# Performance work log

Measured on AMD Instinct MI355X. Metric: run time of the kernel, lower is better.

The kernel has to match this reference:

```python
import jax, jax.numpy as jnp
import numpy as np
from jax import lax

PAD_IDX = 9182


def setup_inputs() -> dict:
    key = jax.random.key(0)
    ks = jax.random.split(key, 16)
    B, S = 16, 256
    V, E, H, SH = 32000, 512, 1024, 1024
    sc = 0.05
    embed = jax.random.normal(ks[0], (V, E), jnp.float32) * sc
    embed = embed.at[PAD_IDX].set(0.0)  # padding_idx row
    inp = {
        "context_encoding": jax.random.normal(ks[1], (B, 1, SH), jnp.float32),
        "target": jax.random.randint(ks[2], (B, S), 0, V),
        "embed": embed,                                              # embed_in.weight (shared out proj)
        "W_s2d": jax.random.normal(ks[3], (H, SH), jnp.float32) * sc,   # ses_to_dec
        "b_s2d": jax.random.normal(ks[4], (H,), jnp.float32) * sc,
        "W_dec_inf": jax.random.normal(ks[5], (2 * E, H), jnp.float32) * sc,
        "W_ses_inf": jax.random.normal(ks[6], (2 * E, SH), jnp.float32) * sc,
        "W_emb_inf": jax.random.normal(ks[7], (2 * E, E), jnp.float32) * sc,
        "b_emb_inf": jax.random.normal(ks[8], (2 * E,), jnp.float32) * sc,
        "W_ih": jax.random.normal(ks[9], (3 * H, E), jnp.float32) * sc,  # GRU input weights
        "W_hh": jax.random.normal(ks[10], (3 * H, H), jnp.float32) * sc,  # GRU hidden weights
        "b_ih": jax.random.normal(ks[11], (3 * H,), jnp.float32) * sc,
        "b_hh": jax.random.normal(ks[12], (3 * H,), jnp.float32) * sc,
    }
    return inp


def _decode(context_encoding, embed, W_s2d, b_s2d, W_dec_inf, W_ses_inf,
            W_emb_inf, b_emb_inf, W_ih, W_hh, b_ih, b_hh, target):
    B, S = target.shape
    ctx = context_encoding[:, 0]                    # [B, SH]
    ses_inf = ctx @ W_ses_inf.T                     # [B, 2E]
    h0 = jnp.tanh(ctx @ W_s2d.T + b_s2d)            # [B, H] init decoder hidden

    emb = embed[target]                             # [B, S, E]
    emb_inf = emb @ W_emb_inf.T + b_emb_inf         # [B, S, 2E]
    x_proj = emb @ W_ih.T + b_ih                    # [B, S, 3H] precomputed GRU input gates

    def gru_step(h, xp):
        gh = h @ W_hh.T + b_hh                      # [B, 3H]
        xr, xz, xn = jnp.split(xp, 3, axis=-1)
        hr, hz, hn = jnp.split(gh, 3, axis=-1)
        r = jax.nn.sigmoid(xr + hr)
        z = jax.nn.sigmoid(xz + hz)
        n = jnp.tanh(xn + r * hn)
        h_new = (1.0 - z) * n + z * h
        return h_new, h_new

    _, hs = lax.scan(gru_step, h0, jnp.swapaxes(x_proj, 0, 1))  # [S, B, H]
    hs = jnp.swapaxes(hs, 0, 1)                     # [B, S, H]

    total = hs @ W_dec_inf.T + ses_inf[:, None, :] + emb_inf  # [B, S, 2E]
    mx = total.reshape(B, S, -1, 2).max(axis=-1)    # maxout pairs -> [B, S, E]
    logits = mx @ embed.T                           # shared embedding out proj [B, S, V]
    return logits


def reference(context_encoding, target, embed, W_s2d, b_s2d, W_dec_inf,
              W_ses_inf, W_emb_inf, b_emb_inf, W_ih, W_hh, b_ih, b_hh):
    dec_o = _decode(context_encoding, embed, W_s2d, b_s2d, W_dec_inf,
                    W_ses_inf, W_emb_inf, b_emb_inf, W_ih, W_hh, b_ih, b_hh,
                    target)
    return dec_o
```

## Files before the change

### kernel.cpp

```cpp
#include <hip/hip_runtime.h>

typedef unsigned short u16;
typedef unsigned int u32;
typedef __attribute__((ext_vector_type(8))) __bf16 bf16x8;
typedef __attribute__((ext_vector_type(4))) float f32x4;
typedef __attribute__((ext_vector_type(4))) u32 u32x4;

#define ASYNC16(g, l) __builtin_amdgcn_global_load_lds( \
    (const __attribute__((address_space(1))) unsigned int*)(g), \
    (__attribute__((address_space(3))) unsigned int*)(l), 16, 0, 0)

__device__ __forceinline__ u16 f2bf(float f){
  unsigned u = __float_as_uint(f);
  unsigned r = u + 0x7fffu + ((u >> 16) & 1u);
  return (u16)(r >> 16);
}

__global__ __launch_bounds__(256) void f2bf_kernel(const float* __restrict__ in,
                                                   u16* __restrict__ out, int n){
  int i = (blockIdx.x * 256 + threadIdx.x) * 8;
  if (i >= n) return;
  float4 a = *(const float4*)&in[i];
  float4 b = *(const float4*)&in[i + 4];
  u16 r[8] = {f2bf(a.x), f2bf(a.y), f2bf(a.z), f2bf(a.w),
              f2bf(b.x), f2bf(b.y), f2bf(b.z), f2bf(b.w)};
  *(uint4*)&out[i] = *(const uint4*)r;
}

__global__ __launch_bounds__(256) void ctx_kernel(const float* __restrict__ ctx,
    const float* __restrict__ Wses, const float* __restrict__ Ws2d,
    const float* __restrict__ bs2d, float* __restrict__ sesinf,
    float* __restrict__ h0f, u16* __restrict__ h0bf){
  int id = blockIdx.x * 4 + (threadIdx.x >> 6);
  int lane = threadIdx.x & 63;
  int n = id & 1023, b = (id >> 10) & 15, mat = id >> 14;
  const float* w = (mat ? Ws2d : Wses) + (size_t)n * 1024;
  const float* x = ctx + (size_t)b * 1024;
  float v = 0.f;
  #pragma unroll 4
  for (int k = lane; k < 1024; k += 64) v += x[k] * w[k];
  #pragma unroll
  for (int off = 32; off; off >>= 1) v += __shfl_down(v, off);
  if (lane == 0){
    if (mat == 0) sesinf[b * 1024 + n] = v;
    else {
      float t = tanhf(v + bs2d[n]);
      h0f[b * 1024 + n] = t;
      h0bf[b * 1024 + n] = f2bf(t);
    }
  }
}

__global__ void gather_kernel(const int* __restrict__ target,
                              const u16* __restrict__ embedBF, u16* __restrict__ embBF){
  int i = blockIdx.x;
  int t = target[i];
  int lane = threadIdx.x;
  *(uint4*)&embBF[(size_t)i * 512 + lane * 8] =
      *(const uint4*)&embedBF[(size_t)t * 512 + lane * 8];
}

template<int EPI, int SWZ>
__global__ __launch_bounds__(256) void gemm_bt(
    const u16* __restrict__ A, const u16* __restrict__ B, float* __restrict__ C,
    int M, int N, int K,
    const float* __restrict__ bias, const float* __restrict__ add0,
    const float* __restrict__ add1, u16* __restrict__ mxout)
{
  __shared__ u16 sA[2][128 * 32];
  __shared__ u16 sB[2][128 * 32];
  int bx = blockIdx.x, by = blockIdx.y;
  if (SWZ){
    int nwg = gridDim.x * gridDim.y;
    int wg = by * gridDim.x + bx;
    int q = nwg >> 3;
    int nw = (wg & 7) * q + (wg >> 3);
    bx = nw % gridDim.x; by = nw / gridDim.x;
  }
  const int n0 = bx * 128;
  const int m0 = by * 128;
  const int tid = threadIdx.x;
  const int lane = tid & 63;
  const int wid = tid >> 6;
  const int wm = (wid >> 1) * 64, wn = (wid & 1) * 64;
  const int l15 = lane & 15, kg = (lane >> 4) * 8;
  (void)M;

  f32x4 zero = {0.f, 0.f, 0.f, 0.f};
  f32x4 acc[4][4];
  #pragma unroll
  for (int m = 0; m < 4; m++)
    #pragma unroll
    for (int n = 0; n < 4; n++) acc[m][n] = zero;

  auto stage = [&](int buf, int kk){
    const u16* Ab = A + (size_t)m0 * K + kk;
    const u16* Bb = B + (size_t)n0 * K + kk;
    #pragma unroll
    for (int j = 0; j < 2; j++){
      int c = j * 256 + tid;
      ASYNC16(Ab + (size_t)(c >> 2) * K + (c & 3) * 8, &sA[buf][c * 8]);
    }
    #pragma unroll
    for (int j = 0; j < 2; j++){
      int c = j * 256 + tid;
      ASYNC16(Bb + (size_t)(c >> 2) * K + (c & 3) * 8, &sB[buf][c * 8]);
    }
  };

  stage(0, 0);
  int cur = 0;
  for (int kk = 0; kk < K; kk += 32){
    __syncthreads();
    if (kk + 32 < K) stage(cur ^ 1, kk + 32);
    bf16x8 af[4], bf_[4];
    #pragma unroll
    for (int m = 0; m < 4; m++)
      af[m] = *(const bf16x8*)&sA[cur][(wm + m * 16 + l15) * 32 + kg];
    #pragma unroll
    for (int n = 0; n < 4; n++)
      bf_[n] = *(const bf16x8*)&sB[cur][(wn + n * 16 + l15) * 32 + kg];
    #pragma unroll
    for (int m = 0; m < 4; m++)
      #pragma unroll
      for (int n = 0; n < 4; n++)
        acc[m][n] = __builtin_amdgcn_mfma_f32_16x16x32_bf16(af[m], bf_[n], acc[m][n], 0, 0, 0);
    cur ^= 1;
  }

  const int rb = m0 + wm + (lane >> 4) * 4;
  const int cb = n0 + wn + l15;
  #pragma unroll
  for (int m = 0; m < 4; m++){
    #pragma unroll
    for (int n = 0; n < 4; n++){
      #pragma unroll
      for (int i = 0; i < 4; i++){
        int row = rb + m * 16 + i;
        int col = cb + n * 16;
        float v = acc[m][n][i];
        if (EPI == 1) v += bias[col];
        if (EPI == 2 || EPI == 3)
          v += add0[(row >> 8) * N + col] + add1[(size_t)row * N + col];
        if (EPI == 3){
          float w = __shfl_xor(v, 1);
          if ((l15 & 1) == 0)
            mxout[(size_t)row * (N >> 1) + (col >> 1)] = f2bf(fmaxf(v, w));
        } else {
          C[(size_t)row * N + col] = v;
        }
      }
    }
  }
}

#define GRU_NWG 64
#define GRU_LDS 136192

__global__ __launch_bounds__(256) void gru_kernel(
    const u16* __restrict__ WhhBF, const float* __restrict__ bhh,
    const float* __restrict__ xproj, const float* __restrict__ h0f,
    const u16* __restrict__ h0bf, u16* __restrict__ hsBF, int* flags)
{
  extern __shared__ char smem[];
  u16*  Wl   = (u16*)smem;
  u16*  hb   = Wl + 48 * 1032;
  float* gbuf = (float*)(smem + 132096);
  float* hown = gbuf + 3 * 256;

  const int g = blockIdx.x;
  const int j0 = g * 16;
  const int tid = threadIdx.x;
  const int lane = tid & 63;
  const int wid = tid >> 6;
  const int bb = tid >> 4, jj = tid & 15;

  for (int c = tid; c < 48 * 128; c += 256){
    int r = c >> 7, cg = (c & 127) * 8;
    int gate = r >> 4, n = r & 15;
    *(uint4*)&Wl[r * 1032 + cg] =
        *(const uint4*)&WhhBF[(size_t)(gate * 1024 + j0 + n) * 1024 + cg];
  }
  hown[bb * 16 + jj] = h0f[bb * 1024 + j0 + jj];
  const float bh0 = bhh[j0 + jj];
  const float bh1 = bhh[1024 + j0 + jj];
  const float bh2 = bhh[2048 + j0 + jj];
  u32* hs32 = (u32*)hsBF;
  __syncthreads();

  for (int s = 0; s < 256; ++s){
    if (s == 0){
      #pragma unroll
      for (int k = 0; k < 8; k++){
        int c = tid + k * 256;
        int b = c >> 7, cg = (c & 127) * 8;
        *(uint4*)&hb[b * 1032 + cg] = *(const uint4*)&h0bf[b * 1024 + cg];
      }
    } else {
      u32x4 r[8];
      #pragma unroll
      for (int k = 0; k < 8; k++){
        int c = tid + k * 256;
        int b = c >> 7, cg = (c & 127) * 8;
        const u16* src = &hsBF[(size_t)((b << 8) + s - 1) * 1024 + cg];
        asm volatile("global_load_dwordx4 %0, %1, off sc1"
                     : "=v"(r[k]) : "v"(src) : "memory");
      }
      asm volatile("s_waitcnt vmcnt(0)" ::: "memory");
      __builtin_amdgcn_sched_barrier(0);
      #pragma unroll
      for (int k = 0; k < 8; k++){
        int c = tid + k * 256;
        int b = c >> 7, cg = (c & 127) * 8;
        *(u32x4*)&hb[b * 1032 + cg] = r[k];
      }
    }

    const float* xp = xproj + ((size_t)(bb << 8) + s) * 3072;
    float xr = xp[j0 + jj], xz = xp[1024 + j0 + jj], xn = xp[2048 + j0 + jj];
    __syncthreads();

    if (wid < 3){
      f32x4 acc0 = {0.f, 0.f, 0.f, 0.f};
      f32x4 acc1 = {0.f, 0.f, 0.f, 0.f};
      const int l15 = lane & 15, kg = (lane >> 4) * 8;
      const u16* wrow = &Wl[(wid * 16 + l15) * 1032];
      const u16* hrow = &hb[l15 * 1032];
      #pragma unroll 8
      for (int kk = 0; kk < 1024; kk += 64){
        bf16x8 a0 = *(const bf16x8*)&hrow[kk + kg];
        bf16x8 w0 = *(const bf16x8*)&wrow[kk + kg];
        acc0 = __builtin_amdgcn_mfma_f32_16x16x32_bf16(a0, w0, acc0, 0, 0, 0);
        bf16x8 a1 = *(const bf16x8*)&hrow[kk + 32 + kg];
        bf16x8 w1 = *(const bf16x8*)&wrow[kk + 32 + kg];
        acc1 = __builtin_amdgcn_mfma_f32_16x16x32_bf16(a1, w1, acc1, 0, 0, 0);
      }
      #pragma unroll
      for (int i = 0; i < 4; ++i)
        gbuf[wid * 256 + ((lane >> 4) * 4 + i) * 16 + l15] = acc0[i] + acc1[i];
    }
    __syncthreads();

    {
      float hr = gbuf[0 * 256 + bb * 16 + jj] + bh0;
      float hz = gbuf[1 * 256 + bb * 16 + jj] + bh1;
      float hn = gbuf[2 * 256 + bb * 16 + jj] + bh2;
      float r = 1.f / (1.f + __expf(-(xr + hr)));
      float z = 1.f / (1.f + __expf(-(xz + hz)));
      float nn = tanhf(xn + r * hn);
      float hnew = (1.f - z) * nn + z * hown[bb * 16 + jj];
      hown[bb * 16 + jj] = hnew;
      float hnext = __shfl_down(hnew, 1);
      if ((jj & 1) == 0){
        u32 pack = (u32)f2bf(hnew) | ((u32)f2bf(hnext) << 16);
        size_t e = (size_t)((bb << 8) + s) * 1024 + j0 + jj;
        __hip_atomic_store(&hs32[e >> 1], pack, __ATOMIC_RELAXED,
                           __HIP_MEMORY_SCOPE_AGENT);
      }
    }

    if (s < 255){
      asm volatile("s_waitcnt vmcnt(0)" ::: "memory");
      __syncthreads();
      if (tid == 0)
        __hip_atomic_store(&flags[g * 32], s + 1, __ATOMIC_RELAXED,
                           __HIP_MEMORY_SCOPE_AGENT);
      if (wid == 0){
        while (__hip_atomic_load(&flags[lane * 32], __ATOMIC_RELAXED,
                                 __HIP_MEMORY_SCOPE_AGENT) <= s)
          __builtin_amdgcn_s_sleep(1);
      }
      __syncthreads();
    }
  }
}

extern "C" void kernel_launch(void* const* d_in, const int* in_sizes, int n_in,
                              void* d_out, int out_size, void* d_ws, size_t ws_size,
                              hipStream_t stream)
{
  const float* ctx    = (const float*)d_in[0];
  const int*   target = (const int*)d_in[1];
  const float* embed  = (const float*)d_in[2];
  const float* Ws2d   = (const float*)d_in[3];
  const float* bs2d   = (const float*)d_in[4];
  const float* Wdec   = (const float*)d_in[5];
  const float* Wses   = (const float*)d_in[6];
  const float* Wemb   = (const float*)d_in[7];
  const float* bemb   = (const float*)d_in[8];
  const float* Wih    = (const float*)d_in[9];
  const float* Whh    = (const float*)d_in[10];
  const float* bih    = (const float*)d_in[11];
  const float* bhh    = (const float*)d_in[12];
  float* out = (float*)d_out;

  char* ws = (char*)d_ws;
  size_t off = 0;
  auto alloc = [&](size_t bytes)->char*{
    char* p = ws + off; off += (bytes + 255) & ~(size_t)255; return p;
  };
  u16*   embedBF = (u16*)alloc(32000ull * 512 * 2);
  u16*   WihBF   = (u16*)alloc(3072ull * 512 * 2);
  u16*   WembBF  = (u16*)alloc(1024ull * 512 * 2);
  u16*   WdecBF  = (u16*)alloc(1024ull * 1024 * 2);
  u16*   WhhBF   = (u16*)alloc(3072ull * 1024 * 2);
  u16*   embBF   = (u16*)alloc(4096ull * 512 * 2);
  float* xproj   = (float*)alloc(4096ull * 3072 * 4);
  float* embinf  = (float*)alloc(4096ull * 1024 * 4);
  float* sesinf  = (float*)alloc(16ull * 1024 * 4);
  float* h0f     = (float*)alloc(16ull * 1024 * 4);
  u16*   h0bf    = (u16*)alloc(16ull * 1024 * 2);
  u16*   hsBF    = (u16*)alloc(4096ull * 1024 * 2);
  u16*   mxBF    = (u16*)alloc(4096ull * 512 * 2);
  int*   flags   = (int*)alloc(16384);
  (void)ws_size; (void)in_sizes; (void)n_in; (void)out_size;

  hipFuncSetAttribute((const void*)gru_kernel,
                      hipFuncAttributeMaxDynamicSharedMemorySize, GRU_LDS);
  hipMemsetAsync(flags, 0, 16384, stream);

  auto conv = [&](const float* in, u16* o, size_t n){
    f2bf_kernel<<<dim3((unsigned)((n / 8 + 255) / 256)), 256, 0, stream>>>(in, o, (int)n);
  };
  conv(embed, embedBF, 32000ull * 512);
  conv(Wih,   WihBF,   3072ull * 512);
  conv(Wemb,  WembBF,  1024ull * 512);
  conv(Wdec,  WdecBF,  1024ull * 1024);
  conv(Whh,   WhhBF,   3072ull * 1024);

  ctx_kernel<<<8192, 256, 0, stream>>>(ctx, Wses, Ws2d, bs2d, sesinf, h0f, h0bf);
  gather_kernel<<<4096, 64, 0, stream>>>(target, embedBF, embBF);

  gemm_bt<1,0><<<dim3(3072 / 128, 4096 / 128), 256, 0, stream>>>(
      embBF, WihBF, xproj, 4096, 3072, 512, bih, nullptr, nullptr, nullptr);
  gemm_bt<1,0><<<dim3(1024 / 128, 4096 / 128), 256, 0, stream>>>(
      embBF, WembBF, embinf, 4096, 1024, 512, bemb, nullptr, nullptr, nullptr);

  gru_kernel<<<GRU_NWG, 256, GRU_LDS, stream>>>(WhhBF, bhh, xproj, h0f, h0bf, hsBF, flags);

  gemm_bt<3,0><<<dim3(1024 / 128, 4096 / 128), 256, 0, stream>>>(
      hsBF, WdecBF, nullptr, 4096, 1024, 1024, nullptr, sesinf, embinf, mxBF);

  gemm_bt<0,1><<<dim3(32000 / 128, 4096 / 128), 256, 0, stream>>>(
      mxBF, embedBF, out, 4096, 32000, 512, nullptr, nullptr, nullptr, nullptr);
}
```

Before: 1.323 ms.

## Restructure GRU recurrence into 16 large workgroups reading W_hh from global

The persistent GRU kernel drops from 64 workgroups of 256 threads to 16 workgroups of 1024 threads, each owning 64 hidden units instead of 16. The weight slice is no longer staged in LDS; each MFMA wave reads its W_hh rows straight from global memory (cache) at every step. The goal is to cut the number of workgroups in the per-step cross-workgroup flag barrier and the redundant hidden-state loads. The cost is re-reading the weights from L2 every step instead of LDS, and far fewer CUs doing the matvec.

```diff
diff --git a/kernel.cpp b/kernel.cpp
--- a/kernel.cpp
+++ b/kernel.cpp
@@ -154,53 +154,48 @@
   }
 }
 
-#define GRU_NWG 64
-#define GRU_LDS 136192
-
-__global__ __launch_bounds__(256) void gru_kernel(
+#define GRU_NWG 16
+
+__global__ __launch_bounds__(1024) void gru_kernel(
     const u16* __restrict__ WhhBF, const float* __restrict__ bhh,
     const float* __restrict__ xproj, const float* __restrict__ h0f,
     const u16* __restrict__ h0bf, u16* __restrict__ hsBF, int* flags)
 {
-  extern __shared__ char smem[];
-  u16*  Wl   = (u16*)smem;
-  u16*  hb   = Wl + 48 * 1032;
-  float* gbuf = (float*)(smem + 132096);
-  float* hown = gbuf + 3 * 256;
+  __shared__ u16   hb[16 * 1032];
+  __shared__ float gbuf[12 * 256];
+  __shared__ float hown[16 * 64];
 
   const int g = blockIdx.x;
-  const int j0 = g * 16;
+  const int j0 = g * 64;
   const int tid = threadIdx.x;
   const int lane = tid & 63;
   const int wid = tid >> 6;
-  const int bb = tid >> 4, jj = tid & 15;
-
-  for (int c = tid; c < 48 * 128; c += 256){
-    int r = c >> 7, cg = (c & 127) * 8;
-    int gate = r >> 4, n = r & 15;
-    *(uint4*)&Wl[r * 1032 + cg] =
-        *(const uint4*)&WhhBF[(size_t)(gate * 1024 + j0 + n) * 1024 + cg];
-  }
-  hown[bb * 16 + jj] = h0f[bb * 1024 + j0 + jj];
+  const int bb = wid;
+  const int jj = lane;
+  const int l15 = lane & 15, kh = lane >> 4;
+
+  hown[bb * 64 + jj] = h0f[bb * 1024 + j0 + jj];
   const float bh0 = bhh[j0 + jj];
   const float bh1 = bhh[1024 + j0 + jj];
   const float bh2 = bhh[2048 + j0 + jj];
+  const u16* wr = WhhBF +
+      (size_t)((wid >> 2) * 1024 + j0 + (wid & 3) * 16 + l15) * 1024;
   u32* hs32 = (u32*)hsBF;
   __syncthreads();
 
   for (int s = 0; s < 256; ++s){
     if (s == 0){
       #pragma unroll
-      for (int k = 0; k < 8; k++){
-        int c = tid + k * 256;
+      for (int k = 0; k < 2; k++){
+        int c = tid + k * 1024;
         int b = c >> 7, cg = (c & 127) * 8;
         *(uint4*)&hb[b * 1032 + cg] = *(const uint4*)&h0bf[b * 1024 + cg];
       }
     } else {
-      u32x4 r[8];
-      #pragma unroll
-      for (int k = 0; k < 8; k++){
-        int c = tid + k * 256;
+      u32x4 r[2];
+      #pragma unroll
+      for (int k = 0; k < 2; k++){
+        int c = tid + k * 1024;
         int b = c >> 7, cg = (c & 127) * 8;
         const u16* src = &hsBF[(size_t)((b << 8) + s - 1) * 1024 + cg];
         asm volatile("global_load_dwordx4 %0, %1, off sc1"
@@ -209,8 +204,8 @@
       asm volatile("s_waitcnt vmcnt(0)" ::: "memory");
       __builtin_amdgcn_sched_barrier(0);
       #pragma unroll
-      for (int k = 0; k < 8; k++){
-        int c = tid + k * 256;
+      for (int k = 0; k < 2; k++){
+        int c = tid + k * 1024;
         int b = c >> 7, cg = (c & 127) * 8;
         *(u32x4*)&hb[b * 1032 + cg] = r[k];
       }
@@ -220,36 +215,37 @@
     float xr = xp[j0 + jj], xz = xp[1024 + j0 + jj], xn = xp[2048 + j0 + jj];
     __syncthreads();
 
-    if (wid < 3){
+    if (wid < 12){
       f32x4 acc0 = {0.f, 0.f, 0.f, 0.f};
       f32x4 acc1 = {0.f, 0.f, 0.f, 0.f};
-      const int l15 = lane & 15, kg = (lane >> 4) * 8;
-      const u16* wrow = &Wl[(wid * 16 + l15) * 1032];
+      const int kh8 = kh * 8;
       const u16* hrow = &hb[l15 * 1032];
-      #pragma unroll 8
+      #pragma unroll 4
       for (int kk = 0; kk < 1024; kk += 64){
-        bf16x8 a0 = *(const bf16x8*)&hrow[kk + kg];
-        bf16x8 w0 = *(const bf16x8*)&wrow[kk + kg];
+        bf16x8 a0 = *(const bf16x8*)&hrow[kk + kh8];
+        bf16x8 w0 = *(const bf16x8*)&wr[kk + kh8];
         acc0 = __builtin_amdgcn_mfma_f32_16x16x32_bf16(a0, w0, acc0, 0, 0, 0);
-        bf16x8 a1 = *(const bf16x8*)&hrow[kk + 32 + kg];
-        bf16x8 w1 = *(const bf16x8*)&wrow[kk + 32 + kg];
+        bf16x8 a1 = *(const bf16x8*)&hrow[kk + 32 + kh8];
+        bf16x8 w1 = *(const bf16x8*)&wr[kk + 32 + kh8];
         acc1 = __builtin_amdgcn_mfma_f32_16x16x32_bf16(a1, w1, acc1, 0, 0, 0);
       }
       #pragma unroll
       for (int i = 0; i < 4; ++i)
-        gbuf[wid * 256 + ((lane >> 4) * 4 + i) * 16 + l15] = acc0[i] + acc1[i];
+        gbuf[wid * 256 + (kh * 4 + i) * 16 + l15] = acc0[i] + acc1[i];
     }
     __syncthreads();
 
     {
-      float hr = gbuf[0 * 256 + bb * 16 + jj] + bh0;
-      float hz = gbuf[1 * 256 + bb * 16 + jj] + bh1;
-      float hn = gbuf[2 * 256 + bb * 16 + jj] + bh2;
+      int tc = (jj >> 4);
+      int ic = bb * 16 + (jj & 15);
+      float hr = gbuf[(0 * 4 + tc) * 256 + ic] + bh0;
+      float hz = gbuf[(1 * 4 + tc) * 256 + ic] + bh1;
+      float hn = gbuf[(2 * 4 + tc) * 256 + ic] + bh2;
       float r = 1.f / (1.f + __expf(-(xr + hr)));
       float z = 1.f / (1.f + __expf(-(xz + hz)));
       float nn = tanhf(xn + r * hn);
-      float hnew = (1.f - z) * nn + z * hown[bb * 16 + jj];
-      hown[bb * 16 + jj] = hnew;
+      float hnew = (1.f - z) * nn + z * hown[bb * 64 + jj];
+      hown[bb * 64 + jj] = hnew;
       float hnext = __shfl_down(hnew, 1);
       if ((jj & 1) == 0){
         u32 pack = (u32)f2bf(hnew) | ((u32)f2bf(hnext) << 16);
@@ -265,7 +261,7 @@
       if (tid == 0)
         __hip_atomic_store(&flags[g * 32], s + 1, __ATOMIC_RELAXED,
                            __HIP_MEMORY_SCOPE_AGENT);
-      if (wid == 0){
+      if (wid == 0 && lane < GRU_NWG){
         while (__hip_atomic_load(&flags[lane * 32], __ATOMIC_RELAXED,
                                  __HIP_MEMORY_SCOPE_AGENT) <= s)
           __builtin_amdgcn_s_sleep(1);
@@ -315,8 +311,6 @@
   int*   flags   = (int*)alloc(16384);
   (void)ws_size; (void)in_sizes; (void)n_in; (void)out_size;
 
-  hipFuncSetAttribute((const void*)gru_kernel,
-                      hipFuncAttributeMaxDynamicSharedMemorySize, GRU_LDS);
   hipMemsetAsync(flags, 0, 16384, stream);
 
   auto conv = [&](const float* in, u16* o, size_t n){
@@ -336,7 +330,7 @@
   gemm_bt<1,0><<<dim3(1024 / 128, 4096 / 128), 256, 0, stream>>>(
       embBF, WembBF, embinf, 4096, 1024, 512, bemb, nullptr, nullptr, nullptr);
 
-  gru_kernel<<<GRU_NWG, 256, GRU_LDS, stream>>>(WhhBF, bhh, xproj, h0f, h0bf, hsBF, flags);
+  gru_kernel<<<GRU_NWG, 1024, 0, stream>>>(WhhBF, bhh, xproj, h0f, h0bf, hsBF, flags);
 
   gemm_bt<3,0><<<dim3(1024 / 128, 4096 / 128), 256, 0, stream>>>(
       hsBF, WdecBF, nullptr, 4096, 1024, 1024, nullptr, sesinf, embinf, mxBF);
```

Measured after the change: 3.676 ms. +177.8%, slower.

## Split GRU recurrent matvec K dimension across 12 waves per block

Applied to the files above, without the earlier changes.

The GRU kernel now launches 1024 threads per block instead of 256. The per-step hidden-state matvec splits K=1024 into four chunks, so 12 waves each compute one gate and one K quarter. Partial sums land in a larger gbuf and are reduced by the first 256 threads before the gate math. This shortens the serial MFMA chain on the latency-bound recurrence, at the cost of extra LDS, more partial-sum reads and heavier block-wide barriers.

```diff
diff --git a/kernel.cpp b/kernel.cpp
--- a/kernel.cpp
+++ b/kernel.cpp
@@ -155,9 +155,9 @@
 }
 
 #define GRU_NWG 64
-#define GRU_LDS 136192
-
-__global__ __launch_bounds__(256) void gru_kernel(
+#define GRU_LDS 145408
+
+__global__ __launch_bounds__(1024) void gru_kernel(
     const u16* __restrict__ WhhBF, const float* __restrict__ bhh,
     const float* __restrict__ xproj, const float* __restrict__ h0f,
     const u16* __restrict__ h0bf, u16* __restrict__ hsBF, int* flags)
@@ -166,41 +166,45 @@
   u16*  Wl   = (u16*)smem;
   u16*  hb   = Wl + 48 * 1032;
   float* gbuf = (float*)(smem + 132096);
-  float* hown = gbuf + 3 * 256;
+  float* hown = gbuf + 12 * 256;
 
   const int g = blockIdx.x;
   const int j0 = g * 16;
   const int tid = threadIdx.x;
   const int lane = tid & 63;
   const int wid = tid >> 6;
-  const int bb = tid >> 4, jj = tid & 15;
-
-  for (int c = tid; c < 48 * 128; c += 256){
+  const int l15 = lane & 15, kh8 = (lane >> 4) * 8;
+
+  for (int c = tid; c < 48 * 128; c += 1024){
     int r = c >> 7, cg = (c & 127) * 8;
     int gate = r >> 4, n = r & 15;
     *(uint4*)&Wl[r * 1032 + cg] =
         *(const uint4*)&WhhBF[(size_t)(gate * 1024 + j0 + n) * 1024 + cg];
   }
-  hown[bb * 16 + jj] = h0f[bb * 1024 + j0 + jj];
-  const float bh0 = bhh[j0 + jj];
-  const float bh1 = bhh[1024 + j0 + jj];
-  const float bh2 = bhh[2048 + j0 + jj];
+  const int bb = (tid & 255) >> 4, jj = tid & 15;
+  float bh0 = 0.f, bh1 = 0.f, bh2 = 0.f;
+  if (tid < 256){
+    hown[bb * 16 + jj] = h0f[bb * 1024 + j0 + jj];
+    bh0 = bhh[j0 + jj];
+    bh1 = bhh[1024 + j0 + jj];
+    bh2 = bhh[2048 + j0 + jj];
+  }
   u32* hs32 = (u32*)hsBF;
   __syncthreads();
 
   for (int s = 0; s < 256; ++s){
     if (s == 0){
       #pragma unroll
-      for (int k = 0; k < 8; k++){
-        int c = tid + k * 256;
+      for (int k = 0; k < 2; k++){
+        int c = tid + k * 1024;
         int b = c >> 7, cg = (c & 127) * 8;
         *(uint4*)&hb[b * 1032 + cg] = *(const uint4*)&h0bf[b * 1024 + cg];
       }
     } else {
-      u32x4 r[8];
-      #pragma unroll
-      for (int k = 0; k < 8; k++){
-        int c = tid + k * 256;
+      u32x4 r[2];
+      #pragma unroll
+      for (int k = 0; k < 2; k++){
+        int c = tid + k * 1024;
         int b = c >> 7, cg = (c & 127) * 8;
         const u16* src = &hsBF[(size_t)((b << 8) + s - 1) * 1024 + cg];
         asm volatile("global_load_dwordx4 %0, %1, off sc1"
@@ -209,30 +213,33 @@
       asm volatile("s_waitcnt vmcnt(0)" ::: "memory");
       __builtin_amdgcn_sched_barrier(0);
       #pragma unroll
-      for (int k = 0; k < 8; k++){
-        int c = tid + k * 256;
+      for (int k = 0; k < 2; k++){
+        int c = tid + k * 1024;
         int b = c >> 7, cg = (c & 127) * 8;
         *(u32x4*)&hb[b * 1032 + cg] = r[k];
       }
     }
 
-    const float* xp = xproj + ((size_t)(bb << 8) + s) * 3072;
-    float xr = xp[j0 + jj], xz = xp[1024 + j0 + jj], xn = xp[2048 + j0 + jj];
+    float xr = 0.f, xz = 0.f, xn = 0.f;
+    if (tid < 256){
+      const float* xp = xproj + ((size_t)(bb << 8) + s) * 3072;
+      xr = xp[j0 + jj]; xz = xp[1024 + j0 + jj]; xn = xp[2048 + j0 + jj];
+    }
     __syncthreads();
 
-    if (wid < 3){
+    if (wid < 12){
+      const int gate = wid >> 2, Koff = (wid & 3) * 256;
       f32x4 acc0 = {0.f, 0.f, 0.f, 0.f};
       f32x4 acc1 = {0.f, 0.f, 0.f, 0.f};
-      const int l15 = lane & 15, kg = (lane >> 4) * 8;
-      const u16* wrow = &Wl[(wid * 16 + l15) * 1032];
-      const u16* hrow = &hb[l15 * 1032];
-      #pragma unroll 8
-      for (int kk = 0; kk < 1024; kk += 64){
-        bf16x8 a0 = *(const bf16x8*)&hrow[kk + kg];
-        bf16x8 w0 = *(const bf16x8*)&wrow[kk + kg];
+      const u16* wrow = &Wl[(gate * 16 + l15) * 1032 + Koff];
+      const u16* hrow = &hb[l15 * 1032 + Koff];
+      #pragma unroll
+      for (int kk = 0; kk < 256; kk += 64){
+        bf16x8 a0 = *(const bf16x8*)&hrow[kk + kh8];
+        bf16x8 w0 = *(const bf16x8*)&wrow[kk + kh8];
         acc0 = __builtin_amdgcn_mfma_f32_16x16x32_bf16(a0, w0, acc0, 0, 0, 0);
-        bf16x8 a1 = *(const bf16x8*)&hrow[kk + 32 + kg];
-        bf16x8 w1 = *(const bf16x8*)&wrow[kk + 32 + kg];
+        bf16x8 a1 = *(const bf16x8*)&hrow[kk + 32 + kh8];
+        bf16x8 w1 = *(const bf16x8*)&wrow[kk + 32 + kh8];
         acc1 = __builtin_amdgcn_mfma_f32_16x16x32_bf16(a1, w1, acc1, 0, 0, 0);
       }
       #pragma unroll
@@ -241,10 +248,14 @@
     }
     __syncthreads();
 
-    {
-      float hr = gbuf[0 * 256 + bb * 16 + jj] + bh0;
-      float hz = gbuf[1 * 256 + bb * 16 + jj] + bh1;
-      float hn = gbuf[2 * 256 + bb * 16 + jj] + bh2;
+    if (tid < 256){
+      int ic = bb * 16 + jj;
+      float hr = gbuf[0 * 256 + ic] + gbuf[1 * 256 + ic] +
+                 gbuf[2 * 256 + ic] + gbuf[3 * 256 + ic] + bh0;
+      float hz = gbuf[4 * 256 + ic] + gbuf[5 * 256 + ic] +
+                 gbuf[6 * 256 + ic] + gbuf[7 * 256 + ic] + bh1;
+      float hn = gbuf[8 * 256 + ic] + gbuf[9 * 256 + ic] +
+                 gbuf[10 * 256 + ic] + gbuf[11 * 256 + ic] + bh2;
       float r = 1.f / (1.f + __expf(-(xr + hr)));
       float z = 1.f / (1.f + __expf(-(xz + hz)));
       float nn = tanhf(xn + r * hn);
@@ -336,7 +347,7 @@
   gemm_bt<1,0><<<dim3(1024 / 128, 4096 / 128), 256, 0, stream>>>(
       embBF, WembBF, embinf, 4096, 1024, 512, bemb, nullptr, nullptr, nullptr);
 
-  gru_kernel<<<GRU_NWG, 256, GRU_LDS, stream>>>(WhhBF, bhh, xproj, h0f, h0bf, hsBF, flags);
+  gru_kernel<<<GRU_NWG, 1024, GRU_LDS, stream>>>(WhhBF, bhh, xproj, h0f, h0bf, hsBF, flags);
 
   gemm_bt<3,0><<<dim3(1024 / 128, 4096 / 128), 256, 0, stream>>>(
       hsBF, WdecBF, nullptr, 4096, 1024, 1024, nullptr, sesinf, embinf, mxBF);
```

Result: faster. 1.159 ms (-12.4%).
